# Optimization experiments

Measured on AMD Instinct MI355X. Metric: run time of the kernel, lower is better.

## Reference

```python
import jax, jax.numpy as jnp
import numpy as np

NUM_HEADS = 16


def sinusoidal_pe(N, C, dtype=jnp.float32):
    # matches the numpy construction in get_positional_encoding
    pos = jnp.arange(N, dtype=dtype)[:, None]                  # [N,1]
    dims = jnp.arange(C)                                        # [C]
    rates = 1.0 / jnp.power(jnp.asarray(10000.0, dtype), (2 * (dims // 2)).astype(dtype) / C)
    ang = pos * rates                                           # [N,C]
    pe = jnp.where(dims % 2 == 0, jnp.sin(ang), jnp.cos(ang))
    return pe.astype(dtype)


def setup_inputs() -> dict:
    key = jax.random.key(0)
    k1, k2, k3 = jax.random.split(key, 3)
    B, N, C = 4, 2048, 1024
    inputs = jax.random.normal(k1, (B, N, C), dtype=jnp.float32)
    mask_mat = jax.random.uniform(k2, (B, N), dtype=jnp.float32)
    # Glorot-uniform qkv kernel [C, 3C]
    limit = float(np.sqrt(6.0 / (C + 3 * C)))
    W_qkv = jax.random.uniform(k3, (C, 3 * C), dtype=jnp.float32, minval=-limit, maxval=limit)
    return {"inputs": inputs, "mask_mat": mask_mat, "W_qkv": W_qkv}


def reference(inputs, mask_mat, W_qkv):
    B, N, C = inputs.shape
    H = NUM_HEADS
    hd = C // H
    scale = hd ** (-0.5)

    # additive mask: -(m outer m), broadcast over heads
    neg_mask = -(mask_mat[:, :, None] * mask_mat[:, None, :])   # [B,N,N]

    x = inputs + sinusoidal_pe(N, C, inputs.dtype)              # APE
    qkv = jnp.einsum('bnc,cd->bnd', x, W_qkv)                   # [B,N,3C]
    qkv = qkv.reshape(B, N, 3, H, hd).transpose(2, 0, 3, 1, 4)  # [3,B,H,N,hd]
    q, k, v = qkv[0], qkv[1], qkv[2]

    attn = jnp.einsum('bhnd,bhmd->bhnm', q, k) * scale          # [B,H,N,N]
    attn = attn + neg_mask[:, None, :, :]
    attn = jax.nn.softmax(attn, axis=-1)
    out = jnp.einsum('bhnm,bhmd->bhnd', attn, v)                # [B,H,N,hd]
    return out.transpose(0, 2, 1, 3).reshape(B, N, C)
```

## Files before the change

kernel.cpp:

```cpp
#include <hip/hip_runtime.h>
#include <hip/hip_bf16.h>

typedef unsigned short u16;
typedef __bf16 bf16x8 __attribute__((ext_vector_type(8)));
typedef float floatx4 __attribute__((ext_vector_type(4)));

#define B_ 4
#define N_ 2048
#define C_ 1024
#define H_ 16
#define HD_ 64

__device__ __forceinline__ float b2f(u16 u) {
    union { float f; unsigned int i; } v; v.i = ((unsigned int)u) << 16; return v.f;
}
__device__ __forceinline__ u16 f2b(float f) {
    union { float f; unsigned int i; } v; v.f = f;
    unsigned int i = v.i;
    unsigned int r = i + 0x7FFFu + ((i >> 16) & 1u);
    return (u16)(r >> 16);
}
__device__ __forceinline__ unsigned int pk2(float a, float b) {
    __hip_bfloat162 t = __float22bfloat162_rn(float2{a, b});
    unsigned int u; __builtin_memcpy(&u, &t, 4); return u;
}
__device__ __forceinline__ void async16(const u16* g, u16* l) {
    __builtin_amdgcn_global_load_lds((const __attribute__((address_space(1))) unsigned int*)g,
                                     (__attribute__((address_space(3))) unsigned int*)l,
                                     16, 0, 0);
}

__global__ __launch_bounds__(256) void pe_add_kernel(const float* __restrict__ in,
                                                     u16* __restrict__ x) {
    int idx = blockIdx.x * 256 + threadIdx.x;
    int cp  = idx & 511;
    int row = idx >> 9;
    int n   = row & (N_ - 1);
    float r = exp2f(-13.287712379549449f * ((float)cp * (1.0f / 512.0f)));
    float ang = (float)n * r;
    float s, c;
    sincosf(ang, &s, &c);
    float2 pr = ((const float2*)in)[idx];
    unsigned int o = ((unsigned int)f2b(pr.y + c) << 16) | (unsigned int)f2b(pr.x + s);
    ((unsigned int*)x)[idx] = o;
}

__global__ __launch_bounds__(256) void wt_kernel(const float* __restrict__ W,
                                                 u16* __restrict__ Wt) {
    __shared__ u16 tile[32][33];
    int bx = blockIdx.x;
    int by = blockIdx.y;
    int tx = threadIdx.x & 31;
    int ty = threadIdx.x >> 5;
    for (int i = 0; i < 32; i += 8)
        tile[ty + i][tx] = f2b(W[(size_t)(by * 32 + ty + i) * 3072 + bx * 32 + tx]);
    __syncthreads();
    for (int i = 0; i < 32; i += 8)
        Wt[(size_t)(bx * 32 + ty + i) * 1024 + by * 32 + tx] = tile[tx][ty + i];
}

__global__ __launch_bounds__(256) void qkv_gemm_kernel(const u16* __restrict__ X,
                                                       const u16* __restrict__ Wt,
                                                       u16* __restrict__ q,
                                                       u16* __restrict__ k,
                                                       u16* __restrict__ vt) {
    __shared__ u16 As[128 * 32];
    __shared__ u16 Bs[128 * 32];
    int tid  = threadIdx.x;
    int wave = tid >> 6, lane = tid & 63, l15 = lane & 15, quad = lane >> 4;
    int m0 = blockIdx.x * 128;
    int n0 = blockIdx.y * 128;
    int wm = (wave & 1) * 64;
    int wn = (wave >> 1) * 64;

    floatx4 acc[4][4];
    for (int i = 0; i < 4; i++)
        for (int j = 0; j < 4; j++)
            acc[i][j] = floatx4{0.f, 0.f, 0.f, 0.f};

    int rowOff = wave * 32 + (lane >> 2);
    int colOff = (lane & 3) * 8;
    const u16* gA = X  + (size_t)(m0 + rowOff) * 1024 + colOff;
    const u16* gB = Wt + (size_t)(n0 + rowOff) * 1024 + colOff;
    u16* lA = As + wave * 1024;
    u16* lB = Bs + wave * 1024;

    for (int k0 = 0; k0 < 1024; k0 += 32) {
        __syncthreads();
        async16(gA + k0,             lA);
        async16(gA + k0 + 16 * 1024, lA + 512);
        async16(gB + k0,             lB);
        async16(gB + k0 + 16 * 1024, lB + 512);
        __syncthreads();

        bf16x8 af[4], bf[4];
        for (int i = 0; i < 4; i++)
            af[i] = *(const bf16x8*)(As + (wm + i * 16 + l15) * 32 + quad * 8);
        for (int j = 0; j < 4; j++)
            bf[j] = *(const bf16x8*)(Bs + (wn + j * 16 + l15) * 32 + quad * 8);
        for (int i = 0; i < 4; i++)
            for (int j = 0; j < 4; j++)
                acc[i][j] = __builtin_amdgcn_mfma_f32_16x16x32_bf16(af[i], bf[j], acc[i][j], 0, 0, 0);
    }

    const float QSC = 0.125f * 1.44269504f;
    for (int i = 0; i < 4; i++) {
        int gm   = m0 + wm + i * 16 + quad * 4;
        int b    = gm >> 11;
        int nloc = gm & 2047;
        for (int j = 0; j < 4; j++) {
            int gn    = n0 + wn + j * 16 + l15;
            int which = gn >> 10;
            int cc    = gn & 1023;
            int h     = cc >> 6;
            int d     = cc & 63;
            size_t bh = (size_t)(b * 16 + h);
            if (which == 2) {
                ushort4 w4;
                w4.x = f2b(acc[i][j][0]);
                w4.y = f2b(acc[i][j][1]);
                w4.z = f2b(acc[i][j][2]);
                w4.w = f2b(acc[i][j][3]);
                *(ushort4*)(vt + (bh * 64 + d) * 2048 + nloc) = w4;
            } else {
                u16* dst = (which == 0) ? q : k;
                float sc = (which == 0) ? QSC : 1.0f;
                for (int r = 0; r < 4; r++)
                    dst[(bh * 2048 + nloc + r) * 64 + d] = f2b(acc[i][j][r] * sc);
            }
        }
    }
}

__global__ __launch_bounds__(256, 4) void attn_kernel(const u16* __restrict__ q,
                                                      const u16* __restrict__ k,
                                                      const u16* __restrict__ vt,
                                                      const float* __restrict__ mask,
                                                      float* __restrict__ out) {
    __shared__ u16 Ks[64 * 72];
    __shared__ u16 Vs[64 * 72];
    __shared__ u16 Ps[4][32 * 72];

    int tid  = threadIdx.x;
    int wave = tid >> 6, lane = tid & 63, l15 = lane & 15, quad = lane >> 4;
    int bh = blockIdx.y, b = bh >> 4, h = bh & 15;
    size_t base = (size_t)bh * (N_ * 64);
    int q0 = blockIdx.x * 128 + wave * 32;
    const float* mkb = mask + b * N_;

    bf16x8 qf[2][2];
    for (int s = 0; s < 2; s++)
        for (int dc = 0; dc < 2; dc++)
            qf[s][dc] = *(const bf16x8*)(q + base + (size_t)(q0 + s * 16 + l15) * 64 + dc * 32 + quad * 8);

    const float L2E = 1.44269504f;
    float nmq[2];
    nmq[0] = -L2E * mkb[q0 + l15];
    nmq[1] = -L2E * mkb[q0 + 16 + l15];

    floatx4 acc[2][4];
    for (int s = 0; s < 2; s++)
        for (int dt = 0; dt < 4; dt++)
            acc[s][dt] = floatx4{0.f, 0.f, 0.f, 0.f};
    float lp[2] = {0.f, 0.f};

    int r_st = tid >> 2;
    int c_st = (tid & 3) * 16;
    u16* Pw = Ps[wave];

    for (int kt = 0; kt < N_; kt += 64) {
        int4 ka = *(const int4*)(k  + base + (size_t)(kt + r_st) * 64 + c_st);
        int4 kb = *(const int4*)(k  + base + (size_t)(kt + r_st) * 64 + c_st + 8);
        int4 va = *(const int4*)(vt + ((size_t)bh * 64 + r_st) * 2048 + kt + c_st);
        int4 vb = *(const int4*)(vt + ((size_t)bh * 64 + r_st) * 2048 + kt + c_st + 8);
        float4 mkv[4];
        for (int t = 0; t < 4; t++)
            mkv[t] = *(const float4*)(mkb + kt + t * 16 + quad * 4);
        __syncthreads();
        *(int4*)(Ks + r_st * 72 + c_st)     = ka;
        *(int4*)(Ks + r_st * 72 + c_st + 8) = kb;
        *(int4*)(Vs + r_st * 72 + c_st)     = va;
        *(int4*)(Vs + r_st * 72 + c_st + 8) = vb;
        __syncthreads();

        for (int t = 0; t < 4; t++) {
            bf16x8 kf0 = *(const bf16x8*)(Ks + (t * 16 + l15) * 72 + quad * 8);
            bf16x8 kf1 = *(const bf16x8*)(Ks + (t * 16 + l15) * 72 + 32 + quad * 8);
            for (int s = 0; s < 2; s++) {
                floatx4 sa = floatx4{0.f, 0.f, 0.f, 0.f};
                sa = __builtin_amdgcn_mfma_f32_16x16x32_bf16(kf0, qf[s][0], sa, 0, 0, 0);
                sa = __builtin_amdgcn_mfma_f32_16x16x32_bf16(kf1, qf[s][1], sa, 0, 0, 0);
                float p0 = exp2f(fmaf(nmq[s], mkv[t].x, sa[0]));
                float p1 = exp2f(fmaf(nmq[s], mkv[t].y, sa[1]));
                float p2 = exp2f(fmaf(nmq[s], mkv[t].z, sa[2]));
                float p3 = exp2f(fmaf(nmq[s], mkv[t].w, sa[3]));
                lp[s] += (p0 + p1) + (p2 + p3);
                uint2 w; w.x = pk2(p0, p1); w.y = pk2(p2, p3);
                *(uint2*)(Pw + (s * 16 + l15) * 72 + t * 16 + quad * 4) = w;
            }
        }

        bf16x8 pf[2][2];
        for (int s = 0; s < 2; s++) {
            pf[s][0] = *(const bf16x8*)(Pw + (s * 16 + l15) * 72 + quad * 8);
            pf[s][1] = *(const bf16x8*)(Pw + (s * 16 + l15) * 72 + 32 + quad * 8);
        }
        for (int dt = 0; dt < 4; dt++) {
            bf16x8 vf0 = *(const bf16x8*)(Vs + (dt * 16 + l15) * 72 + quad * 8);
            bf16x8 vf1 = *(const bf16x8*)(Vs + (dt * 16 + l15) * 72 + 32 + quad * 8);
            for (int s = 0; s < 2; s++) {
                acc[s][dt] = __builtin_amdgcn_mfma_f32_16x16x32_bf16(pf[s][0], vf0, acc[s][dt], 0, 0, 0);
                acc[s][dt] = __builtin_amdgcn_mfma_f32_16x16x32_bf16(pf[s][1], vf1, acc[s][dt], 0, 0, 0);
            }
        }
    }

    for (int s = 0; s < 2; s++) {
        float lf = lp[s];
        lf += __shfl_xor(lf, 16);
        lf += __shfl_xor(lf, 32);
        float invl = 1.0f / lf;
        for (int r = 0; r < 4; r++) {
            float ir = __shfl(invl, (lane & 48) | (quad * 4 + r));
            int qrow = q0 + s * 16 + quad * 4 + r;
            float* orow = out + ((size_t)(b * N_ + qrow)) * C_ + h * 64;
            for (int dt = 0; dt < 4; dt++)
                orow[dt * 16 + l15] = acc[s][dt][r] * ir;
        }
    }
}

extern "C" void kernel_launch(void* const* d_in, const int* in_sizes, int n_in,
                              void* d_out, int out_size, void* d_ws, size_t ws_size,
                              hipStream_t stream) {
    const float* inp  = (const float*)d_in[0];
    const float* mask = (const float*)d_in[1];
    const float* W    = (const float*)d_in[2];
    float* out = (float*)d_out;

    char* ws = (char*)d_ws;
    u16* x  = (u16*)ws;
    u16* Wt = (u16*)(ws + 16777216);
    u16* q  = (u16*)(ws + 23068672);
    u16* k  = q + 8388608;
    u16* vt = k + 8388608;

    pe_add_kernel<<<16384, 256, 0, stream>>>(inp, x);
    wt_kernel<<<dim3(96, 32), 256, 0, stream>>>(W, Wt);
    qkv_gemm_kernel<<<dim3(64, 24), 256, 0, stream>>>(x, Wt, q, k, vt);
    attn_kernel<<<dim3(16, 64), 256, 0, stream>>>(q, k, vt, mask, out);
}
```

Before: 281.0 us.

## Load K and V MFMA fragments directly from global memory, dropping LDS staging

The attention kernel no longer stages K and V tiles into shared memory with two block-wide barriers per iteration. Each wave now reads its MFMA operand fragments for K and transposed V straight from global memory, and loads the mask per sub-tile. This removes the LDS round-trip and the __syncthreads stalls, and also frees LDS so more blocks can be resident. In exchange each of the four waves re-reads the same K/V data, which relies on L1/L2 caching, and the global loads are no longer software-prefetched ahead of the compute.

Result: slower. 409.9 us (+45.8%).

```diff
diff --git a/kernel.cpp b/kernel.cpp
--- a/kernel.cpp
+++ b/kernel.cpp
@@ -137,8 +137,6 @@
                                                       const u16* __restrict__ vt,
                                                       const float* __restrict__ mask,
                                                       float* __restrict__ out) {
-    __shared__ u16 Ks[64 * 72];
-    __shared__ u16 Vs[64 * 72];
     __shared__ u16 Ps[4][32 * 72];
 
     int tid  = threadIdx.x;
@@ -164,36 +162,24 @@
             acc[s][dt] = floatx4{0.f, 0.f, 0.f, 0.f};
     float lp[2] = {0.f, 0.f};
 
-    int r_st = tid >> 2;
-    int c_st = (tid & 3) * 16;
     u16* Pw = Ps[wave];
+    const u16* kfb = k  + base + (size_t)l15 * 64 + quad * 8;
+    const u16* vfb = vt + ((size_t)bh * 64 + l15) * 2048 + quad * 8;
 
     for (int kt = 0; kt < N_; kt += 64) {
-        int4 ka = *(const int4*)(k  + base + (size_t)(kt + r_st) * 64 + c_st);
-        int4 kb = *(const int4*)(k  + base + (size_t)(kt + r_st) * 64 + c_st + 8);
-        int4 va = *(const int4*)(vt + ((size_t)bh * 64 + r_st) * 2048 + kt + c_st);
-        int4 vb = *(const int4*)(vt + ((size_t)bh * 64 + r_st) * 2048 + kt + c_st + 8);
-        float4 mkv[4];
-        for (int t = 0; t < 4; t++)
-            mkv[t] = *(const float4*)(mkb + kt + t * 16 + quad * 4);
-        __syncthreads();
-        *(int4*)(Ks + r_st * 72 + c_st)     = ka;
-        *(int4*)(Ks + r_st * 72 + c_st + 8) = kb;
-        *(int4*)(Vs + r_st * 72 + c_st)     = va;
-        *(int4*)(Vs + r_st * 72 + c_st + 8) = vb;
-        __syncthreads();
-
         for (int t = 0; t < 4; t++) {
-            bf16x8 kf0 = *(const bf16x8*)(Ks + (t * 16 + l15) * 72 + quad * 8);
-            bf16x8 kf1 = *(const bf16x8*)(Ks + (t * 16 + l15) * 72 + 32 + quad * 8);
+            const u16* kp = kfb + (size_t)(kt + t * 16) * 64;
+            bf16x8 kf0 = *(const bf16x8*)(kp);
+            bf16x8 kf1 = *(const bf16x8*)(kp + 32);
+            float4 mkv = *(const float4*)(mkb + kt + t * 16 + quad * 4);
             for (int s = 0; s < 2; s++) {
                 floatx4 sa = floatx4{0.f, 0.f, 0.f, 0.f};
                 sa = __builtin_amdgcn_mfma_f32_16x16x32_bf16(kf0, qf[s][0], sa, 0, 0, 0);
                 sa = __builtin_amdgcn_mfma_f32_16x16x32_bf16(kf1, qf[s][1], sa, 0, 0, 0);
-                float p0 = exp2f(fmaf(nmq[s], mkv[t].x, sa[0]));
-                float p1 = exp2f(fmaf(nmq[s], mkv[t].y, sa[1]));
-                float p2 = exp2f(fmaf(nmq[s], mkv[t].z, sa[2]));
-                float p3 = exp2f(fmaf(nmq[s], mkv[t].w, sa[3]));
+                float p0 = exp2f(fmaf(nmq[s], mkv.x, sa[0]));
+                float p1 = exp2f(fmaf(nmq[s], mkv.y, sa[1]));
+                float p2 = exp2f(fmaf(nmq[s], mkv.z, sa[2]));
+                float p3 = exp2f(fmaf(nmq[s], mkv.w, sa[3]));
                 lp[s] += (p0 + p1) + (p2 + p3);
                 uint2 w; w.x = pk2(p0, p1); w.y = pk2(p2, p3);
                 *(uint2*)(Pw + (s * 16 + l15) * 72 + t * 16 + quad * 4) = w;
@@ -206,8 +192,9 @@
             pf[s][1] = *(const bf16x8*)(Pw + (s * 16 + l15) * 72 + 32 + quad * 8);
         }
         for (int dt = 0; dt < 4; dt++) {
-            bf16x8 vf0 = *(const bf16x8*)(Vs + (dt * 16 + l15) * 72 + quad * 8);
-            bf16x8 vf1 = *(const bf16x8*)(Vs + (dt * 16 + l15) * 72 + 32 + quad * 8);
+            const u16* vp = vfb + (size_t)dt * 16 * 2048 + kt;
+            bf16x8 vf0 = *(const bf16x8*)(vp);
+            bf16x8 vf1 = *(const bf16x8*)(vp + 32);
             for (int s = 0; s < 2; s++) {
                 acc[s][dt] = __builtin_amdgcn_mfma_f32_16x16x32_bf16(pf[s][0], vf0, acc[s][dt], 0, 0, 0);
                 acc[s][dt] = __builtin_amdgcn_mfma_f32_16x16x32_bf16(pf[s][1], vf1, acc[s][dt], 0, 0, 0);
```
